# Performance work log

Hardware: AMD Instinct MI355X
Metric: run time of the kernel (lower is better)

Reference implementation:

```python
import jax, jax.numpy as jnp
import numpy as np

NUM_CLASSES = 32
N = 2_000_000
EPS = jnp.float32(np.finfo(np.float32).eps)  # torch.finfo(torch.float32).eps


def setup_inputs() -> dict:
    key = jax.random.key(0)
    k1, k2 = jax.random.split(key)
    y_true = jax.random.normal(k1, (N, NUM_CLASSES), dtype=jnp.float32)
    y_pred = jax.random.normal(k2, (N, NUM_CLASSES), dtype=jnp.float32)
    confusion_matrix = jnp.zeros((NUM_CLASSES, NUM_CLASSES), dtype=jnp.float32)
    return {"y_true": y_true, "y_pred": y_pred, "confusion_matrix": confusion_matrix}


def reference(y_true, y_pred, confusion_matrix):
    C = confusion_matrix.shape[0]
    # update(): argmax then scatter-accumulate into the confusion matrix
    t = jnp.argmax(y_true, axis=1)  # [N] int
    p = jnp.argmax(y_pred, axis=1)  # [N] int
    flat = t * C + p                # flattened (row, col) index
    hist = jnp.zeros((C * C,), dtype=jnp.float32).at[flat].add(1.0)
    cm = confusion_matrix + hist.reshape(C, C)
    # compute() with average='macro'
    tp = jnp.diag(cm)
    predicted_positives = jnp.sum(cm, axis=0)
    precision_per_class = tp / (predicted_positives + EPS)
    return jnp.mean(precision_per_class)
```

## Files before the change

### kernel.cpp

```cpp
#include <hip/hip_runtime.h>

#define C 32
#define BINS (C * C)
#define NBLOCKS 2048
#define NTHREADS 256
#define ROWS_PER_STEP ((NBLOCKS * NTHREADS) / 8)
#define FLT_EPS 1.1920928955078125e-07f

typedef float v4f __attribute__((ext_vector_type(4)));

__device__ __forceinline__ unsigned long long pack_best4(v4f v, int base) {
    unsigned long long best = 0ull;
    #pragma unroll
    for (int k = 0; k < 4; ++k) {
        unsigned int u = __float_as_uint(v[k]);
        unsigned int key = u ^ ((unsigned int)((int)u >> 31) | 0x80000000u);
        unsigned long long p =
            ((unsigned long long)key << 32) | (unsigned int)(63 - (base + k));
        best = (p > best) ? p : best;
    }
    return best;
}

__global__ __launch_bounds__(NTHREADS) void hist_kernel(
    const float* __restrict__ yt,
    const float* __restrict__ yp,
    unsigned int* __restrict__ partial,
    int N)
{
    __shared__ unsigned int lhist[BINS];
    const int t = threadIdx.x;
    for (int i = t; i < BINS; i += NTHREADS) lhist[i] = 0u;
    __syncthreads();

    const int lane8 = t & 7;
    long long row = (long long)((blockIdx.x * NTHREADS + t) >> 3);
    bool valid = row < N;
    v4f a, b;
    if (valid) {
        a = __builtin_nontemporal_load(((const v4f*)(yt + row * C)) + lane8);
        b = __builtin_nontemporal_load(((const v4f*)(yp + row * C)) + lane8);
    }

    while (valid) {
        const long long nrow = row + ROWS_PER_STEP;
        const bool nvalid = nrow < N;
        v4f na, nb;
        if (nvalid) {
            na = __builtin_nontemporal_load(((const v4f*)(yt + nrow * C)) + lane8);
            nb = __builtin_nontemporal_load(((const v4f*)(yp + nrow * C)) + lane8);
        }

        unsigned long long bt = pack_best4(a, lane8 * 4);
        unsigned long long bp = pack_best4(b, lane8 * 4);
        #pragma unroll
        for (int m = 1; m < 8; m <<= 1) {
            unsigned long long ot = __shfl_xor(bt, m);
            bt = (ot > bt) ? ot : bt;
            unsigned long long op = __shfl_xor(bp, m);
            bp = (op > bp) ? op : bp;
        }
        if (lane8 == 0) {
            const int ti = 63 - (int)(bt & 63ull);
            const int pi = 63 - (int)(bp & 63ull);
            atomicAdd(&lhist[ti * C + pi], 1u);
        }

        row = nrow; valid = nvalid; a = na; b = nb;
    }

    __syncthreads();
    if (t < 32) {
        unsigned int cs = 0;
        #pragma unroll
        for (int i = 0; i < C; ++i) cs += lhist[i * C + t];
        partial[(size_t)blockIdx.x * 64 + t] = cs;
    } else if (t < 64) {
        const int j = t - 32;
        partial[(size_t)blockIdx.x * 64 + t] = lhist[j * C + j];
    }
}

__global__ __launch_bounds__(1024) void finalize_kernel(
    const unsigned int* __restrict__ partial,
    const float* __restrict__ cm_in,
    float* __restrict__ out)
{
    __shared__ float sums[16][64];
    const int tid = threadIdx.x;
    const int col = tid & 63;
    const int kg = tid >> 6;

    unsigned int s = 0;
    #pragma unroll 8
    for (int k = kg * (NBLOCKS / 16); k < (kg + 1) * (NBLOCKS / 16); ++k)
        s += partial[(size_t)k * 64 + col];
    sums[kg][col] = (float)s;
    __syncthreads();

    if (tid < 64) {
        float tot = 0.0f;
        #pragma unroll
        for (int g = 0; g < 16; ++g) tot += sums[g][tid];
        sums[0][tid] = tot;
    }
    __syncthreads();

    if (tid < C) {
        const int j = tid;
        float pp = sums[0][j];
        float tp = sums[0][C + j];
        float cmcol = 0.0f;
        #pragma unroll
        for (int i = 0; i < C; ++i) cmcol += cm_in[i * C + j];
        pp += cmcol;
        tp += cm_in[j * C + j];
        float prec = tp / (pp + FLT_EPS);
        #pragma unroll
        for (int m = 1; m < C; m <<= 1) prec += __shfl_xor(prec, m);
        if (j == 0) out[0] = prec * (1.0f / (float)C);
    }
}

extern "C" void kernel_launch(void* const* d_in, const int* in_sizes, int n_in,
                              void* d_out, int out_size, void* d_ws, size_t ws_size,
                              hipStream_t stream)
{
    const float* yt = (const float*)d_in[0];
    const float* yp = (const float*)d_in[1];
    const float* cm = (const float*)d_in[2];
    float* out = (float*)d_out;
    const int N = in_sizes[0] / C;

    unsigned int* partial = (unsigned int*)d_ws;

    hist_kernel<<<NBLOCKS, NTHREADS, 0, stream>>>(yt, yp, partial, N);
    finalize_kernel<<<1, 1024, 0, stream>>>(partial, cm, out);
}
```

Measured before the change: 461.5 us.

## Use DPP float max/min argmax and process two row groups per iteration

```diff
diff --git a/kernel.cpp b/kernel.cpp
--- a/kernel.cpp
+++ b/kernel.cpp
@@ -4,22 +4,39 @@
 #define BINS (C * C)
 #define NBLOCKS 2048
 #define NTHREADS 256
-#define ROWS_PER_STEP ((NBLOCKS * NTHREADS) / 8)
+#define GROUP_STRIDE ((NBLOCKS * NTHREADS) / 8)
+#define STRIDE2 (2 * GROUP_STRIDE)
 #define FLT_EPS 1.1920928955078125e-07f
 
 typedef float v4f __attribute__((ext_vector_type(4)));
 
-__device__ __forceinline__ unsigned long long pack_best4(v4f v, int base) {
-    unsigned long long best = 0ull;
-    #pragma unroll
-    for (int k = 0; k < 4; ++k) {
-        unsigned int u = __float_as_uint(v[k]);
-        unsigned int key = u ^ ((unsigned int)((int)u >> 31) | 0x80000000u);
-        unsigned long long p =
-            ((unsigned long long)key << 32) | (unsigned int)(63 - (base + k));
-        best = (p > best) ? p : best;
-    }
-    return best;
+template <int CTRL>
+__device__ __forceinline__ float dpp_maxf(float x) {
+    float o = __int_as_float(__builtin_amdgcn_update_dpp(
+        0, __float_as_int(x), CTRL, 0xF, 0xF, true));
+    return fmaxf(x, o);
+}
+template <int CTRL>
+__device__ __forceinline__ unsigned int dpp_minu(unsigned int x) {
+    unsigned int o = (unsigned int)__builtin_amdgcn_update_dpp(
+        0, (int)x, CTRL, 0xF, 0xF, true);
+    return x < o ? x : o;
+}
+
+__device__ __forceinline__ int group_argmax(v4f v, int base) {
+    float m = fmaxf(fmaxf(v.x, v.y), fmaxf(v.z, v.w));
+    m = dpp_maxf<0xB1>(m);
+    m = dpp_maxf<0x4E>(m);
+    m = dpp_maxf<0x141>(m);
+    unsigned int idx = 255u;
+    idx = (v.w == m) ? (unsigned int)(base + 3) : idx;
+    idx = (v.z == m) ? (unsigned int)(base + 2) : idx;
+    idx = (v.y == m) ? (unsigned int)(base + 1) : idx;
+    idx = (v.x == m) ? (unsigned int)(base + 0) : idx;
+    idx = dpp_minu<0xB1>(idx);
+    idx = dpp_minu<0x4E>(idx);
+    idx = dpp_minu<0x141>(idx);
+    return (int)idx;
 }
 
 __global__ __launch_bounds__(NTHREADS) void hist_kernel(
@@ -34,39 +51,50 @@
     __syncthreads();
 
     const int lane8 = t & 7;
-    long long row = (long long)((blockIdx.x * NTHREADS + t) >> 3);
-    bool valid = row < N;
-    v4f a, b;
-    if (valid) {
-        a = __builtin_nontemporal_load(((const v4f*)(yt + row * C)) + lane8);
-        b = __builtin_nontemporal_load(((const v4f*)(yp + row * C)) + lane8);
+    const int base = lane8 * 4;
+    const float* pt = yt + base;
+    const float* pp = yp + base;
+
+    long long r0 = (long long)((blockIdx.x * NTHREADS + t) >> 3);
+    long long r1 = r0 + GROUP_STRIDE;
+    bool v0 = r0 < N;
+    bool v1 = r1 < N;
+    v4f a0, b0, a1, b1;
+    if (v0) {
+        a0 = __builtin_nontemporal_load((const v4f*)(pt + r0 * C));
+        b0 = __builtin_nontemporal_load((const v4f*)(pp + r0 * C));
+    }
+    if (v1) {
+        a1 = __builtin_nontemporal_load((const v4f*)(pt + r1 * C));
+        b1 = __builtin_nontemporal_load((const v4f*)(pp + r1 * C));
     }
 
-    while (valid) {
-        const long long nrow = row + ROWS_PER_STEP;
-        const bool nvalid = nrow < N;
-        v4f na, nb;
-        if (nvalid) {
-            na = __builtin_nontemporal_load(((const v4f*)(yt + nrow * C)) + lane8);
-            nb = __builtin_nontemporal_load(((const v4f*)(yp + nrow * C)) + lane8);
+    while (v0) {
+        const long long n0 = r0 + STRIDE2;
+        const long long n1 = r1 + STRIDE2;
+        const bool nv0 = n0 < N;
+        const bool nv1 = n1 < N;
+        v4f na0, nb0, na1, nb1;
+        if (nv0) {
+            na0 = __builtin_nontemporal_load((const v4f*)(pt + n0 * C));
+            nb0 = __builtin_nontemporal_load((const v4f*)(pp + n0 * C));
+        }
+        if (nv1) {
+            na1 = __builtin_nontemporal_load((const v4f*)(pt + n1 * C));
+            nb1 = __builtin_nontemporal_load((const v4f*)(pp + n1 * C));
         }
 
-        unsigned long long bt = pack_best4(a, lane8 * 4);
-        unsigned long long bp = pack_best4(b, lane8 * 4);
-        #pragma unroll
-        for (int m = 1; m < 8; m <<= 1) {
-            unsigned long long ot = __shfl_xor(bt, m);
-            bt = (ot > bt) ? ot : bt;
-            unsigned long long op = __shfl_xor(bp, m);
-            bp = (op > bp) ? op : bp;
-        }
-        if (lane8 == 0) {
-            const int ti = 63 - (int)(bt & 63ull);
-            const int pi = 63 - (int)(bp & 63ull);
-            atomicAdd(&lhist[ti * C + pi], 1u);
+        const int ti0 = group_argmax(a0, base);
+        const int pi0 = group_argmax(b0, base);
+        if (lane8 == 0) atomicAdd(&lhist[ti0 * C + pi0], 1u);
+        if (v1) {
+            const int ti1 = group_argmax(a1, base);
+            const int pi1 = group_argmax(b1, base);
+            if (lane8 == 1) atomicAdd(&lhist[ti1 * C + pi1], 1u);
         }
 
-        row = nrow; valid = nvalid; a = na; b = nb;
+        r0 = n0; r1 = n1; v0 = nv0; v1 = nv1;
+        a0 = na0; b0 = nb0; a1 = na1; b1 = nb1;
     }
 
     __syncthreads();
```

Measured after the change: 461.5 us. Within noise of the previous version (-0.0%).
